# Optimization experiments

Measured on AMD Instinct MI355X. Metric: run time of the kernel, lower is better.

## Reference

```python
import jax, jax.numpy as jnp
import numpy as np
from jax import lax

T, P, EPS = 8, 3, 1e-5


def setup_inputs() -> dict:
    key = jax.random.key(0)
    ks = jax.random.split(key, 12)
    n, c, h, w = 16, 512, 28, 28
    r = c // 8
    sc = 1.0 / np.sqrt(c).astype(np.float32)
    return {
        "X": jax.random.normal(ks[0], (n * T, c, h, w), jnp.float32),
        "conv1_w": jax.random.normal(ks[1], (r, c, 1, 1, 1), jnp.float32) * 0.05,
        "conv1_b": jnp.zeros((r,), jnp.float32),
        "g1": jnp.ones((r,), jnp.float32),
        "b1": jnp.zeros((r,), jnp.float32),
        "m1": jax.random.normal(ks[2], (r,), jnp.float32) * 0.1,
        "v1": jax.random.uniform(ks[3], (r,), jnp.float32, 0.5, 1.5),
        "conv2_w": jax.random.normal(ks[4], (r, r, 3, 1, 1), jnp.float32) * 0.05,
        "conv2_b": jnp.zeros((r,), jnp.float32),
        "conv3_w": jax.random.normal(ks[5], (P, r, 1, 5, 5), jnp.float32) * 0.05,
        "conv3_b": jnp.zeros((P,), jnp.float32),
        "g2": jnp.ones((P,), jnp.float32),
        "b2": jnp.zeros((P,), jnp.float32),
        "m2": jax.random.normal(ks[6], (P,), jnp.float32) * 0.1,
        "v2": jax.random.uniform(ks[7], (P,), jnp.float32, 0.5, 1.5),
        "gcn0_w": jax.random.normal(ks[8], (c, c), jnp.float32) * sc,
        "gcn1_w": jax.random.normal(ks[9], (c, c), jnp.float32) * sc,
        "att_w": jax.random.normal(ks[10], (1, c), jnp.float32) * sc,
        "att_b": jnp.zeros((1,), jnp.float32),
    }


def _conv3d(x, w, b, pad):
    y = lax.conv_general_dilated(x, w, (1, 1, 1), pad,
                                 dimension_numbers=("NCDHW", "OIDHW", "NCDHW"))
    return y + b[None, :, None, None, None]


def _bn(x, g, b, m, v):
    # eval-mode BatchNorm3d folded into scale/shift
    inv = g * lax.rsqrt(v + EPS)
    return x * inv[None, :, None, None, None] + (b - m * inv)[None, :, None, None, None]


def _lrelu(x):
    return jnp.where(x >= 0, x, 0.05 * x)


def reference(X, conv1_w, conv1_b, g1, b1, m1, v1, conv2_w, conv2_b,
              conv3_w, conv3_b, g2, b2, m2, v2, gcn0_w, gcn1_w, att_w, att_b):
    nt, c, h, w = X.shape
    n = nt // T
    Xr = X.reshape(n, T, c, h, w)
    residual = Xr.mean((3, 4))                          # [n,t,c]
    Xp = jnp.transpose(Xr, (0, 2, 1, 3, 4))             # [n,c,t,h,w]

    # saliency detector
    s = _lrelu(_bn(_conv3d(Xp, conv1_w, conv1_b, [(0, 0)] * 3), g1, b1, m1, v1))
    s = _conv3d(s, conv2_w, conv2_b, [(1, 1), (0, 0), (0, 0)])
    s = _conv3d(s, conv3_w, conv3_b, [(0, 0), (2, 2), (2, 2)])
    s_map = jax.nn.sigmoid(_bn(s, g2, b2, m2, v2))      # [n,P,t,h,w]

    # weighted node pooling (avoids the [n,c,P,t,h,w] broadcast intermediate)
    nodes = jnp.einsum('ncthw,npthw->ntpc', Xp, s_map) / (h * w)
    nodes = nodes.reshape(n, T * P, c)                  # [n,N,c], N=24

    # normalized Laplacian as elementwise outer-product scaling
    A = jnp.einsum('nic,njc->nij', nodes, nodes) / c
    deg = jnp.clip(A.sum(-1), 1e-8, None)
    dinv = deg ** -0.5
    L = dinv[:, :, None] * A * dinv[:, None, :]

    # GCN (2 bias-free layers) + attention readout
    Xg = nodes
    for W in (gcn0_w, gcn1_w):
        Xg = _lrelu(L @ (Xg @ W.T))
    att = jax.nn.softmax(L @ ((Xg + nodes) @ att_w.T) + att_b, axis=1)  # [n,N,1]
    readout = (Xg * att).sum(1)                         # [n,c]
    return jnp.concatenate([readout[:, None, :], residual], axis=1)  # [n,t+1,c]
```

## Files before the change

### kernel.cpp

```cpp
#include <hip/hip_runtime.h>
#include <hip/hip_bf16.h>
#include <math.h>

#define NT 128
#define NB 16
#define TT 8
#define C 512
#define RR 64
#define HW 784
#define HH 28
#define WW 28
#define PP 3
#define NN 24
#define EPS 1e-5f

typedef __attribute__((ext_vector_type(8))) short bh8;
typedef __attribute__((ext_vector_type(4))) float f32x4;

static __device__ inline unsigned short f2bf(float f) {
    __hip_bfloat16 h = __float2bfloat16(f);
    return *(unsigned short*)&h;
}
static __device__ inline float bf2f(unsigned short u) {
    __hip_bfloat16 h;
    *(unsigned short*)&h = u;
    return __bfloat162float(h);
}

__global__ __launch_bounds__(256) void convA_mfma(const float* __restrict__ X,
        const float* __restrict__ W1, const float* __restrict__ cb,
        const float* __restrict__ g, const float* __restrict__ bb,
        const float* __restrict__ m, const float* __restrict__ v,
        float* __restrict__ s1)
{
    __shared__ unsigned short Xh[32 * 72];
    __shared__ unsigned short Xl[32 * 72];
    __shared__ unsigned short Wh[4 * 64 * 8];
    __shared__ unsigned short Wl[4 * 64 * 8];
    __shared__ float sInv[64], sAdd[64], sCb[64];

    const int nt  = blockIdx.y;
    const int hw0 = blockIdx.x * 64;
    const int tid = threadIdx.x;

    if (tid < 64) {
        float inv = g[tid] * rsqrtf(v[tid] + EPS);
        sInv[tid] = inv;
        sAdd[tid] = bb[tid] - m[tid] * inv;
        sCb[tid]  = cb[tid];
    }

    const int sk = tid >> 3;
    const int ss = tid & 7;
    const int wr = tid >> 2;
    const int wj = tid & 3;
    const bool full = (hw0 + 64 <= HW);

    const int wv = tid >> 6;
    const int l  = tid & 63;
    const int gq = l >> 4;
    const int mm16 = l & 15;
    const int xbase = (gq * 8) * 72 + 16 * wv + (mm16 ^ ((gq & 1) << 3));

    f32x4 acc[4];
    #pragma unroll
    for (int i = 0; i < 4; ++i) acc[i] = (f32x4){0.f, 0.f, 0.f, 0.f};

    const float* Xnt = X + (size_t)nt * C * HW;

    for (int k0 = 0; k0 < C; k0 += 32) {
        {
            const float* src = Xnt + (size_t)(k0 + sk) * HW + hw0 + ss * 8;
            float x[8];
            if (full) {
                float4 a = *(const float4*)src;
                float4 b = *(const float4*)(src + 4);
                x[0] = a.x; x[1] = a.y; x[2] = a.z; x[3] = a.w;
                x[4] = b.x; x[5] = b.y; x[6] = b.z; x[7] = b.w;
            } else {
                #pragma unroll
                for (int i = 0; i < 8; ++i) {
                    int hw = hw0 + ss * 8 + i;
                    x[i] = (hw < HW) ? src[i] : 0.f;
                }
            }
            unsigned int hp[4], lp[4];
            #pragma unroll
            for (int i = 0; i < 4; ++i) {
                unsigned short h0 = f2bf(x[2 * i]), h1 = f2bf(x[2 * i + 1]);
                unsigned short l0 = f2bf(x[2 * i] - bf2f(h0));
                unsigned short l1 = f2bf(x[2 * i + 1] - bf2f(h1));
                hp[i] = (unsigned int)h0 | ((unsigned int)h1 << 16);
                lp[i] = (unsigned int)l0 | ((unsigned int)l1 << 16);
            }
            int xoff = sk * 72 + ((ss * 8) ^ (((sk >> 3) & 1) << 3));
            *(uint4*)&Xh[xoff] = make_uint4(hp[0], hp[1], hp[2], hp[3]);
            *(uint4*)&Xl[xoff] = make_uint4(lp[0], lp[1], lp[2], lp[3]);
        }
        {
            const float* wsrc = W1 + (size_t)wr * C + k0 + wj * 8;
            float4 a = *(const float4*)wsrc;
            float4 b = *(const float4*)(wsrc + 4);
            float x[8] = {a.x, a.y, a.z, a.w, b.x, b.y, b.z, b.w};
            unsigned int hp[4], lp[4];
            #pragma unroll
            for (int i = 0; i < 4; ++i) {
                unsigned short h0 = f2bf(x[2 * i]), h1 = f2bf(x[2 * i + 1]);
                unsigned short l0 = f2bf(x[2 * i] - bf2f(h0));
                unsigned short l1 = f2bf(x[2 * i + 1] - bf2f(h1));
                hp[i] = (unsigned int)h0 | ((unsigned int)h1 << 16);
                lp[i] = (unsigned int)l0 | ((unsigned int)l1 << 16);
            }
            int woff = ((wr >> 4) * 64 + (wr & 15) + 16 * wj) * 8;
            *(uint4*)&Wh[woff] = make_uint4(hp[0], hp[1], hp[2], hp[3]);
            *(uint4*)&Wl[woff] = make_uint4(lp[0], lp[1], lp[2], lp[3]);
        }
        __syncthreads();

        union { bh8 v; unsigned short u[8]; } fxh, fxl;
        #pragma unroll
        for (int j = 0; j < 8; ++j) {
            fxh.u[j] = Xh[xbase + j * 72];
            fxl.u[j] = Xl[xbase + j * 72];
        }
        #pragma unroll
        for (int rt = 0; rt < 4; ++rt) {
            bh8 wh = *(const bh8*)&Wh[(rt * 64 + l) * 8];
            bh8 wl = *(const bh8*)&Wl[(rt * 64 + l) * 8];
            acc[rt] = __builtin_amdgcn_mfma_f32_16x16x32_bf16(wh, fxh.v, acc[rt], 0, 0, 0);
            acc[rt] = __builtin_amdgcn_mfma_f32_16x16x32_bf16(wh, fxl.v, acc[rt], 0, 0, 0);
            acc[rt] = __builtin_amdgcn_mfma_f32_16x16x32_bf16(wl, fxh.v, acc[rt], 0, 0, 0);
        }
        __syncthreads();
    }

    const int hw = hw0 + 16 * wv + mm16;
    if (hw < HW) {
        #pragma unroll
        for (int rt = 0; rt < 4; ++rt) {
            #pragma unroll
            for (int reg = 0; reg < 4; ++reg) {
                int r = rt * 16 + 4 * gq + reg;
                float y = (acc[rt][reg] + sCb[r]) * sInv[r] + sAdd[r];
                y = (y >= 0.f) ? y : 0.05f * y;
                s1[((size_t)nt * RR + r) * HW + hw] = y;
            }
        }
    }
}

__global__ __launch_bounds__(256) void convB(const float* __restrict__ s1,
        const float* __restrict__ W2, const float* __restrict__ cb,
        float* __restrict__ s2)
{
    __shared__ float Xs[32][64];
    __shared__ float Ws[32][68];
    const int nt = blockIdx.y;
    const int n = nt >> 3, t = nt & 7;
    const int hw0 = blockIdx.x * 64;
    const int tid = threadIdx.x;
    const int tr = tid & 15, tc = tid >> 4;
    float acc[4][4] = {};

    for (int dt = 0; dt < 3; ++dt) {
        int tp = t + dt - 1;
        if (tp < 0 || tp >= TT) continue;
        const float* Sp = s1 + (size_t)(n * TT + tp) * RR * HW;
        for (int k0 = 0; k0 < RR; k0 += 32) {
            #pragma unroll
            for (int i = 0; i < 8; ++i) {
                int idx = tid + i * 256;
                int kl = idx >> 6, hwl = idx & 63;
                int hw = hw0 + hwl;
                Xs[kl][hwl] = (hw < HW) ? Sp[(k0 + kl) * HW + hw] : 0.f;
            }
            #pragma unroll
            for (int i = 0; i < 8; ++i) {
                int idx = tid + i * 256;
                int kl = idx & 31, r = idx >> 5;
                Ws[kl][r] = W2[r * 192 + (k0 + kl) * 3 + dt];
            }
            __syncthreads();
            #pragma unroll
            for (int k = 0; k < 32; ++k) {
                float4 xv = *(const float4*)&Xs[k][tr * 4];
                float4 wv = *(const float4*)&Ws[k][tc * 4];
                acc[0][0] += xv.x * wv.x; acc[0][1] += xv.x * wv.y;
                acc[0][2] += xv.x * wv.z; acc[0][3] += xv.x * wv.w;
                acc[1][0] += xv.y * wv.x; acc[1][1] += xv.y * wv.y;
                acc[1][2] += xv.y * wv.z; acc[1][3] += xv.y * wv.w;
                acc[2][0] += xv.z * wv.x; acc[2][1] += xv.z * wv.y;
                acc[2][2] += xv.z * wv.z; acc[2][3] += xv.z * wv.w;
                acc[3][0] += xv.w * wv.x; acc[3][1] += xv.w * wv.y;
                acc[3][2] += xv.w * wv.z; acc[3][3] += xv.w * wv.w;
            }
            __syncthreads();
        }
    }
    #pragma unroll
    for (int j = 0; j < 4; ++j) {
        int r = tc * 4 + j;
        float cbr = cb[r];
        #pragma unroll
        for (int i = 0; i < 4; ++i) {
            int hw = hw0 + tr * 4 + i;
            if (hw < HW)
                s2[((size_t)nt * RR + r) * HW + hw] = acc[i][j] + cbr;
        }
    }
}

__global__ __launch_bounds__(256) void convC(const float* __restrict__ s2,
        const float* __restrict__ W3, const float* __restrict__ cb,
        const float* __restrict__ g, const float* __restrict__ bb,
        const float* __restrict__ m, const float* __restrict__ v,
        float* __restrict__ smap)
{
    __shared__ float tile[8][18][36];
    const int nt = blockIdx.y;
    const int half = blockIdx.x;
    const int tid = threadIdx.x;
    const int row0 = half * 14 - 2;
    const int orl = tid / 14;
    const int wsi = tid % 14;
    const int orow = half * 14 + orl;
    const int w0 = wsi * 2;
    float acc[3][2] = {};
    const float* S = s2 + (size_t)nt * RR * HW;

    for (int rc0 = 0; rc0 < RR; rc0 += 8) {
        for (int i = 0; i < 21; ++i) {
            int idx = tid + i * 256;
            if (idx < 5184) {
                int rl = idx / 648;
                int rem = idx - rl * 648;
                int rr = rem / 36;
                int cs = rem - rr * 36;
                int grow = row0 + rr;
                int c = cs - 2;
                float val = 0.f;
                if (grow >= 0 && grow < HH && c >= 0 && c < WW)
                    val = S[(rc0 + rl) * HW + grow * WW + c];
                tile[rl][rr][cs] = val;
            }
        }
        __syncthreads();
        if (tid < 196) {
            #pragma unroll
            for (int rl = 0; rl < 8; ++rl) {
                const float* wr2 = W3 + (rc0 + rl) * 25;
                #pragma unroll
                for (int dh = 0; dh < 5; ++dh) {
                    const float* trow = &tile[rl][orl + dh][w0];
                    float inb[6];
                    #pragma unroll
                    for (int q = 0; q < 6; ++q) inb[q] = trow[q];
                    #pragma unroll
                    for (int dw = 0; dw < 5; ++dw) {
                        float v0 = inb[dw], v1 = inb[dw + 1];
                        #pragma unroll
                        for (int p = 0; p < 3; ++p) {
                            float wv = wr2[p * 1600 + dh * 5 + dw];
                            acc[p][0] += v0 * wv;
                            acc[p][1] += v1 * wv;
                        }
                    }
                }
            }
        }
        __syncthreads();
    }
    if (tid < 196) {
        #pragma unroll
        for (int p = 0; p < 3; ++p) {
            float inv = g[p] / sqrtf(v[p] + EPS);
            float add = bb[p] - m[p] * inv;
            #pragma unroll
            for (int j = 0; j < 2; ++j) {
                float z = (acc[p][j] + cb[p]) * inv + add;
                float sg = 1.f / (1.f + expf(-z));
                smap[((size_t)nt * PP + p) * HW + orow * WW + w0 + j] = sg;
            }
        }
    }
}

__global__ __launch_bounds__(256) void poolD(const float* __restrict__ X,
        const float* __restrict__ smap, float* __restrict__ nodes,
        float* __restrict__ out)
{
    const int tid = threadIdx.x;
    const int lane = tid & 63;
    const int gw = blockIdx.x * 4 + (tid >> 6);
    const int c = gw & 511;
    const int nt = gw >> 9;
    const float4* X4 = (const float4*)(X + ((size_t)nt * C + c) * HW);
    const float4* S0 = (const float4*)(smap + (size_t)nt * PP * HW);
    const float4* S1 = S0 + 196;
    const float4* S2 = S1 + 196;
    float sx = 0.f, a0 = 0.f, a1 = 0.f, a2 = 0.f;
    #pragma unroll
    for (int i = 0; i < 4; ++i) {
        int fi = i * 64 + lane;
        if (fi < 196) {
            float4 x = X4[fi];
            float4 p0 = S0[fi], p1 = S1[fi], p2 = S2[fi];
            sx += x.x + x.y + x.z + x.w;
            a0 += x.x * p0.x + x.y * p0.y + x.z * p0.z + x.w * p0.w;
            a1 += x.x * p1.x + x.y * p1.y + x.z * p1.z + x.w * p1.w;
            a2 += x.x * p2.x + x.y * p2.y + x.z * p2.z + x.w * p2.w;
        }
    }
    #pragma unroll
    for (int off = 32; off >= 1; off >>= 1) {
        sx += __shfl_xor(sx, off);
        a0 += __shfl_xor(a0, off);
        a1 += __shfl_xor(a1, off);
        a2 += __shfl_xor(a2, off);
    }
    if (lane == 0) {
        int n = nt >> 3, t = nt & 7;
        const float s = 1.f / 784.f;
        out[((size_t)n * 9 + 1 + t) * C + c] = sx * s;
        float* nd = nodes + ((size_t)n * NN + t * PP) * C + c;
        nd[0]     = a0 * s;
        nd[C]     = a1 * s;
        nd[2 * C] = a2 * s;
    }
}

__global__ __launch_bounds__(256) void graphL(const float* __restrict__ nodes,
        float* __restrict__ Lg)
{
    __shared__ float4 nds[24][129];
    __shared__ float Amat[24][24];
    __shared__ float dinv[24];
    const int n = blockIdx.x;
    const int tid = threadIdx.x;
    const float4* src = (const float4*)(nodes + (size_t)n * NN * C);
    #pragma unroll
    for (int i = 0; i < 12; ++i) {
        int fi = tid + i * 256;
        int row = fi >> 7, k4 = fi & 127;
        nds[row][k4] = src[row * 128 + k4];
    }
    __syncthreads();
    for (int pair = tid; pair < 576; pair += 256) {
        int i = pair / 24, j = pair - (pair / 24) * 24;
        const float4* ri = &nds[i][0];
        const float4* rj = &nds[j][0];
        float s = 0.f;
        for (int k = 0; k < 128; ++k) {
            float4 a = ri[k], b = rj[k];
            s += a.x * b.x + a.y * b.y + a.z * b.z + a.w * b.w;
        }
        Amat[i][j] = s * (1.f / 512.f);
    }
    __syncthreads();
    if (tid < 24) {
        float d = 0.f;
        for (int j = 0; j < 24; ++j) d += Amat[tid][j];
        d = fmaxf(d, 1e-8f);
        dinv[tid] = 1.f / sqrtf(d);
    }
    __syncthreads();
    for (int pair = tid; pair < 576; pair += 256) {
        int i = pair / 24, j = pair - (pair / 24) * 24;
        Lg[(size_t)n * 576 + pair] = dinv[i] * Amat[i][j] * dinv[j];
    }
}

__global__ __launch_bounds__(256) void gemmG(const float* __restrict__ Xin,
        const float* __restrict__ Wm, float* __restrict__ Y)
{
    __shared__ float Xs[32][36];
    __shared__ float Ws[32][66];
    const int o0 = blockIdx.x * 64;
    const int m0 = blockIdx.y * 32;
    const int tid = threadIdx.x;
    const int tr = tid >> 5;
    const int tc = tid & 31;
    float acc[4][2] = {};

    for (int k0 = 0; k0 < 512; k0 += 32) {
        {
            int ml = tid >> 3, k4 = tid & 7;
            float4 xv = *(const float4*)&Xin[(size_t)(m0 + ml) * 512 + k0 + k4 * 4];
            Xs[k4 * 4 + 0][ml] = xv.x; Xs[k4 * 4 + 1][ml] = xv.y;
            Xs[k4 * 4 + 2][ml] = xv.z; Xs[k4 * 4 + 3][ml] = xv.w;
        }
        #pragma unroll
        for (int i = 0; i < 2; ++i) {
            int idx = tid + i * 256;
            int ol = idx >> 3, k4 = idx & 7;
            float4 wv = *(const float4*)&Wm[(size_t)(o0 + ol) * 512 + k0 + k4 * 4];
            Ws[k4 * 4 + 0][ol] = wv.x; Ws[k4 * 4 + 1][ol] = wv.y;
            Ws[k4 * 4 + 2][ol] = wv.z; Ws[k4 * 4 + 3][ol] = wv.w;
        }
        __syncthreads();
        #pragma unroll
        for (int k = 0; k < 32; ++k) {
            float4 xv = *(const float4*)&Xs[k][tr * 4];
            float2 wv = *(const float2*)&Ws[k][tc * 2];
            acc[0][0] += xv.x * wv.x; acc[0][1] += xv.x * wv.y;
            acc[1][0] += xv.y * wv.x; acc[1][1] += xv.y * wv.y;
            acc[2][0] += xv.z * wv.x; acc[2][1] += xv.z * wv.y;
            acc[3][0] += xv.w * wv.x; acc[3][1] += xv.w * wv.y;
        }
        __syncthreads();
    }
    #pragma unroll
    for (int i2 = 0; i2 < 4; ++i2)
        #pragma unroll
        for (int j = 0; j < 2; ++j)
            Y[(size_t)(m0 + tr * 4 + i2) * 512 + o0 + tc * 2 + j] = acc[i2][j];
}

__global__ __launch_bounds__(256) void applyL(const float* __restrict__ G,
        const float* __restrict__ Lg, float* __restrict__ Xg)
{
    __shared__ float Ls[576];
    const int n = blockIdx.y;
    const int tid = threadIdx.x;
    for (int i = tid; i < 576; i += 256) Ls[i] = Lg[(size_t)n * 576 + i];
    __syncthreads();
    const int o = blockIdx.x * 128 + (tid & 127);
    const int ig = (tid >> 7) * 12;
    float acc[12] = {};
    const float* Gn = G + (size_t)n * NN * 512;
    for (int j = 0; j < 24; ++j) {
        float gv = Gn[j * 512 + o];
        #pragma unroll
        for (int i = 0; i < 12; ++i)
            acc[i] += Ls[(ig + i) * 24 + j] * gv;
    }
    float* Xn = Xg + (size_t)n * NN * 512;
    #pragma unroll
    for (int i = 0; i < 12; ++i) {
        float y = acc[i];
        Xn[(ig + i) * 512 + o] = (y >= 0.f) ? y : 0.05f * y;
    }
}

__global__ __launch_bounds__(256) void attE(const float* __restrict__ Xg,
        const float* __restrict__ nodes, const float* __restrict__ Lg,
        const float* __restrict__ aw, const float* __restrict__ ab,
        float* __restrict__ out)
{
    __shared__ float zs[24], ys[24], att[24], Ls[576];
    const int n = blockIdx.x;
    const int tid = threadIdx.x;
    const int lane = tid & 63, wv = tid >> 6;
    for (int i = tid; i < 576; i += 256) Ls[i] = Lg[(size_t)n * 576 + i];
    const float* Xn = Xg + (size_t)n * NN * 512;
    const float* Nn = nodes + (size_t)n * NN * 512;
    for (int i = wv; i < 24; i += 4) {
        float s = 0.f;
        #pragma unroll
        for (int kk = 0; kk < 8; ++kk) {
            int k = kk * 64 + lane;
            s += (Xn[i * 512 + k] + Nn[i * 512 + k]) * aw[k];
        }
        #pragma unroll
        for (int off = 32; off >= 1; off >>= 1) s += __shfl_xor(s, off);
        if (lane == 0) zs[i] = s;
    }
    __syncthreads();
    if (tid < 24) {
        float y = ab[0];
        for (int j = 0; j < 24; ++j) y += Ls[tid * 24 + j] * zs[j];
        ys[tid] = y;
    }
    __syncthreads();
    if (tid < 64) {
        float vv = (tid < 24) ? ys[tid] : -3.4e38f;
        float mx = vv;
        #pragma unroll
        for (int off = 32; off >= 1; off >>= 1) mx = fmaxf(mx, __shfl_xor(mx, off));
        float e = (tid < 24) ? expf(vv - mx) : 0.f;
        float ssum = e;
        #pragma unroll
        for (int off = 32; off >= 1; off >>= 1) ssum += __shfl_xor(ssum, off);
        if (tid < 24) att[tid] = e / ssum;
    }
    __syncthreads();
    for (int c2 = tid; c2 < 512; c2 += 256) {
        float r = 0.f;
        #pragma unroll
        for (int i = 0; i < 24; ++i) r += Xn[i * 512 + c2] * att[i];
        out[(size_t)n * 9 * 512 + c2] = r;
    }
}

extern "C" void kernel_launch(void* const* d_in, const int* in_sizes, int n_in,
                              void* d_out, int out_size, void* d_ws, size_t ws_size,
                              hipStream_t stream)
{
    const float* X   = (const float*)d_in[0];
    const float* w1  = (const float*)d_in[1];
    const float* b1c = (const float*)d_in[2];
    const float* g1  = (const float*)d_in[3];
    const float* b1  = (const float*)d_in[4];
    const float* m1  = (const float*)d_in[5];
    const float* v1  = (const float*)d_in[6];
    const float* w2  = (const float*)d_in[7];
    const float* b2c = (const float*)d_in[8];
    const float* w3  = (const float*)d_in[9];
    const float* b3c = (const float*)d_in[10];
    const float* g2  = (const float*)d_in[11];
    const float* b2  = (const float*)d_in[12];
    const float* m2  = (const float*)d_in[13];
    const float* v2  = (const float*)d_in[14];
    const float* gw0 = (const float*)d_in[15];
    const float* gw1 = (const float*)d_in[16];
    const float* aw  = (const float*)d_in[17];
    const float* ab  = (const float*)d_in[18];
    float* out = (float*)d_out;

    float* ws    = (float*)d_ws;
    float* s1    = ws;
    float* s2    = s1 + (size_t)NT * RR * HW;
    float* smap  = s2 + (size_t)NT * RR * HW;
    float* nodes = smap + (size_t)NT * PP * HW;
    float* Lg    = nodes + (size_t)NB * NN * C;
    float* gt    = Lg + (size_t)NB * NN * NN;
    float* xa    = gt + (size_t)NB * NN * C;
    float* xb    = xa + (size_t)NB * NN * C;

    convA_mfma<<<dim3(13, NT), 256, 0, stream>>>(X, w1, b1c, g1, b1, m1, v1, s1);
    convB<<<dim3(13, NT), 256, 0, stream>>>(s1, w2, b2c, s2);
    convC<<<dim3(2, NT), 256, 0, stream>>>(s2, w3, b3c, g2, b2, m2, v2, smap);
    poolD<<<dim3(16384), 256, 0, stream>>>(X, smap, nodes, out);
    graphL<<<dim3(NB), 256, 0, stream>>>(nodes, Lg);
    gemmG<<<dim3(8, 12), 256, 0, stream>>>(nodes, gw0, gt);
    applyL<<<dim3(4, NB), 256, 0, stream>>>(gt, Lg, xa);
    gemmG<<<dim3(8, 12), 256, 0, stream>>>(xa, gw1, gt);
    applyL<<<dim3(4, NB), 256, 0, stream>>>(gt, Lg, xb);
    attE<<<dim3(NB), 256, 0, stream>>>(xb, nodes, Lg, aw, ab, out);
}
```

Measured before the change: 599.3 us.

## Move temporal conv to split-bf16 MFMA and restructure 5x5 conv as channel-split sliding window

```diff
diff --git a/kernel.cpp b/kernel.cpp
--- a/kernel.cpp
+++ b/kernel.cpp
@@ -16,14 +16,15 @@
 
 typedef __attribute__((ext_vector_type(8))) short bh8;
 typedef __attribute__((ext_vector_type(4))) float f32x4;
-
-static __device__ inline unsigned short f2bf(float f) {
+typedef unsigned short u16;
+
+static __device__ inline u16 f2bf(float f) {
     __hip_bfloat16 h = __float2bfloat16(f);
-    return *(unsigned short*)&h;
-}
-static __device__ inline float bf2f(unsigned short u) {
+    return *(u16*)&h;
+}
+static __device__ inline float bf2f(u16 u) {
     __hip_bfloat16 h;
-    *(unsigned short*)&h = u;
+    *(u16*)&h = u;
     return __bfloat162float(h);
 }
 
@@ -31,12 +32,12 @@
         const float* __restrict__ W1, const float* __restrict__ cb,
         const float* __restrict__ g, const float* __restrict__ bb,
         const float* __restrict__ m, const float* __restrict__ v,
-        float* __restrict__ s1)
-{
-    __shared__ unsigned short Xh[32 * 72];
-    __shared__ unsigned short Xl[32 * 72];
-    __shared__ unsigned short Wh[4 * 64 * 8];
-    __shared__ unsigned short Wl[4 * 64 * 8];
+        u16* __restrict__ s1h, u16* __restrict__ s1l)
+{
+    __shared__ u16 Xh[32 * 72];
+    __shared__ u16 Xl[32 * 72];
+    __shared__ u16 Wh[4 * 64 * 8];
+    __shared__ u16 Wl[4 * 64 * 8];
     __shared__ float sInv[64], sAdd[64], sCb[64];
 
     const int nt  = blockIdx.y;
@@ -87,9 +88,9 @@
             unsigned int hp[4], lp[4];
             #pragma unroll
             for (int i = 0; i < 4; ++i) {
-                unsigned short h0 = f2bf(x[2 * i]), h1 = f2bf(x[2 * i + 1]);
-                unsigned short l0 = f2bf(x[2 * i] - bf2f(h0));
-                unsigned short l1 = f2bf(x[2 * i + 1] - bf2f(h1));
+                u16 h0 = f2bf(x[2 * i]), h1 = f2bf(x[2 * i + 1]);
+                u16 l0 = f2bf(x[2 * i] - bf2f(h0));
+                u16 l1 = f2bf(x[2 * i + 1] - bf2f(h1));
                 hp[i] = (unsigned int)h0 | ((unsigned int)h1 << 16);
                 lp[i] = (unsigned int)l0 | ((unsigned int)l1 << 16);
             }
@@ -105,9 +106,9 @@
             unsigned int hp[4], lp[4];
             #pragma unroll
             for (int i = 0; i < 4; ++i) {
-                unsigned short h0 = f2bf(x[2 * i]), h1 = f2bf(x[2 * i + 1]);
-                unsigned short l0 = f2bf(x[2 * i] - bf2f(h0));
-                unsigned short l1 = f2bf(x[2 * i + 1] - bf2f(h1));
+                u16 h0 = f2bf(x[2 * i]), h1 = f2bf(x[2 * i + 1]);
+                u16 l0 = f2bf(x[2 * i] - bf2f(h0));
+                u16 l1 = f2bf(x[2 * i + 1] - bf2f(h1));
                 hp[i] = (unsigned int)h0 | ((unsigned int)h1 << 16);
                 lp[i] = (unsigned int)l0 | ((unsigned int)l1 << 16);
             }
@@ -117,7 +118,7 @@
         }
         __syncthreads();
 
-        union { bh8 v; unsigned short u[8]; } fxh, fxl;
+        union { bh8 v; u16 u[8]; } fxh, fxl;
         #pragma unroll
         for (int j = 0; j < 8; ++j) {
             fxh.u[j] = Xh[xbase + j * 72];
@@ -143,146 +144,213 @@
                 int r = rt * 16 + 4 * gq + reg;
                 float y = (acc[rt][reg] + sCb[r]) * sInv[r] + sAdd[r];
                 y = (y >= 0.f) ? y : 0.05f * y;
-                s1[((size_t)nt * RR + r) * HW + hw] = y;
-            }
-        }
-    }
-}
-
-__global__ __launch_bounds__(256) void convB(const float* __restrict__ s1,
-        const float* __restrict__ W2, const float* __restrict__ cb,
-        float* __restrict__ s2)
-{
-    __shared__ float Xs[32][64];
-    __shared__ float Ws[32][68];
-    const int nt = blockIdx.y;
+                size_t idx = ((size_t)nt * RR + r) * HW + hw;
+                u16 h = f2bf(y);
+                s1h[idx] = h;
+                s1l[idx] = f2bf(y - bf2f(h));
+            }
+        }
+    }
+}
+
+__global__ __launch_bounds__(256) void convB_mfma(const u16* __restrict__ s1h,
+        const u16* __restrict__ s1l, const float* __restrict__ W2,
+        const float* __restrict__ cb, float* __restrict__ s2)
+{
+    __shared__ u16 Xh[32 * 72];
+    __shared__ u16 Xl[32 * 72];
+    __shared__ u16 Wh[6 * 4 * 64 * 8];
+    __shared__ u16 Wl[6 * 4 * 64 * 8];
+
+    const int nt  = blockIdx.y;
     const int n = nt >> 3, t = nt & 7;
     const int hw0 = blockIdx.x * 64;
     const int tid = threadIdx.x;
-    const int tr = tid & 15, tc = tid >> 4;
-    float acc[4][4] = {};
+    const bool full = (hw0 + 64 <= HW);
+
+    const int wr = tid >> 2, wj = tid & 3;
+    #pragma unroll
+    for (int dk = 0; dk < 6; ++dk) {
+        int dt = dk >> 1, kc = dk & 1;
+        const float* wsrc = W2 + (size_t)wr * 192 + (kc * 32 + wj * 8) * 3 + dt;
+        float x[8];
+        #pragma unroll
+        for (int i = 0; i < 8; ++i) x[i] = wsrc[i * 3];
+        unsigned int hp[4], lp[4];
+        #pragma unroll
+        for (int i = 0; i < 4; ++i) {
+            u16 h0 = f2bf(x[2 * i]), h1 = f2bf(x[2 * i + 1]);
+            u16 l0 = f2bf(x[2 * i] - bf2f(h0));
+            u16 l1 = f2bf(x[2 * i + 1] - bf2f(h1));
+            hp[i] = (unsigned int)h0 | ((unsigned int)h1 << 16);
+            lp[i] = (unsigned int)l0 | ((unsigned int)l1 << 16);
+        }
+        int woff = dk * 2048 + ((wr >> 4) * 64 + (wr & 15) + 16 * wj) * 8;
+        *(uint4*)&Wh[woff] = make_uint4(hp[0], hp[1], hp[2], hp[3]);
+        *(uint4*)&Wl[woff] = make_uint4(lp[0], lp[1], lp[2], lp[3]);
+    }
+    __syncthreads();
+
+    const int sk = tid >> 3, ss = tid & 7;
+    const int wv = tid >> 6, l = tid & 63;
+    const int gq = l >> 4, mm16 = l & 15;
+    const int xbase = (gq * 8) * 72 + 16 * wv + (mm16 ^ ((gq & 1) << 3));
+    const int xoff = sk * 72 + ((ss * 8) ^ (((sk >> 3) & 1) << 3));
+
+    f32x4 acc[4];
+    #pragma unroll
+    for (int i = 0; i < 4; ++i) acc[i] = (f32x4){0.f, 0.f, 0.f, 0.f};
 
     for (int dt = 0; dt < 3; ++dt) {
         int tp = t + dt - 1;
         if (tp < 0 || tp >= TT) continue;
-        const float* Sp = s1 + (size_t)(n * TT + tp) * RR * HW;
-        for (int k0 = 0; k0 < RR; k0 += 32) {
-            #pragma unroll
-            for (int i = 0; i < 8; ++i) {
-                int idx = tid + i * 256;
-                int kl = idx >> 6, hwl = idx & 63;
-                int hw = hw0 + hwl;
-                Xs[kl][hwl] = (hw < HW) ? Sp[(k0 + kl) * HW + hw] : 0.f;
-            }
-            #pragma unroll
-            for (int i = 0; i < 8; ++i) {
-                int idx = tid + i * 256;
-                int kl = idx & 31, r = idx >> 5;
-                Ws[kl][r] = W2[r * 192 + (k0 + kl) * 3 + dt];
+        const size_t pbase = (size_t)(n * TT + tp) * RR * HW;
+        #pragma unroll
+        for (int kc = 0; kc < 2; ++kc) {
+            const size_t roff = pbase + (size_t)(kc * 32 + sk) * HW + hw0 + ss * 8;
+            uint4 hv, lv;
+            if (full) {
+                hv = *(const uint4*)(s1h + roff);
+                lv = *(const uint4*)(s1l + roff);
+            } else {
+                u16 ha[8], la[8];
+                #pragma unroll
+                for (int i = 0; i < 8; ++i) {
+                    int hw = hw0 + ss * 8 + i;
+                    ha[i] = (hw < HW) ? s1h[roff + i] : (u16)0;
+                    la[i] = (hw < HW) ? s1l[roff + i] : (u16)0;
+                }
+                hv = *(uint4*)ha; lv = *(uint4*)la;
             }
             __syncthreads();
-            #pragma unroll
-            for (int k = 0; k < 32; ++k) {
-                float4 xv = *(const float4*)&Xs[k][tr * 4];
-                float4 wv = *(const float4*)&Ws[k][tc * 4];
-                acc[0][0] += xv.x * wv.x; acc[0][1] += xv.x * wv.y;
-                acc[0][2] += xv.x * wv.z; acc[0][3] += xv.x * wv.w;
-                acc[1][0] += xv.y * wv.x; acc[1][1] += xv.y * wv.y;
-                acc[1][2] += xv.y * wv.z; acc[1][3] += xv.y * wv.w;
-                acc[2][0] += xv.z * wv.x; acc[2][1] += xv.z * wv.y;
-                acc[2][2] += xv.z * wv.z; acc[2][3] += xv.z * wv.w;
-                acc[3][0] += xv.w * wv.x; acc[3][1] += xv.w * wv.y;
-                acc[3][2] += xv.w * wv.z; acc[3][3] += xv.w * wv.w;
-            }
+            *(uint4*)&Xh[xoff] = hv;
+            *(uint4*)&Xl[xoff] = lv;
             __syncthreads();
-        }
-    }
-    #pragma unroll
-    for (int j = 0; j < 4; ++j) {
-        int r = tc * 4 + j;
-        float cbr = cb[r];
-        #pragma unroll
-        for (int i = 0; i < 4; ++i) {
-            int hw = hw0 + tr * 4 + i;
-            if (hw < HW)
-                s2[((size_t)nt * RR + r) * HW + hw] = acc[i][j] + cbr;
-        }
-    }
-}
-
-__global__ __launch_bounds__(256) void convC(const float* __restrict__ s2,
-        const float* __restrict__ W3, const float* __restrict__ cb,
-        const float* __restrict__ g, const float* __restrict__ bb,
-        const float* __restrict__ m, const float* __restrict__ v,
-        float* __restrict__ smap)
-{
-    __shared__ float tile[8][18][36];
-    const int nt = blockIdx.y;
-    const int half = blockIdx.x;
-    const int tid = threadIdx.x;
-    const int row0 = half * 14 - 2;
-    const int orl = tid / 14;
-    const int wsi = tid % 14;
-    const int orow = half * 14 + orl;
-    const int w0 = wsi * 2;
-    float acc[3][2] = {};
-    const float* S = s2 + (size_t)nt * RR * HW;
-
-    for (int rc0 = 0; rc0 < RR; rc0 += 8) {
-        for (int i = 0; i < 21; ++i) {
-            int idx = tid + i * 256;
-            if (idx < 5184) {
-                int rl = idx / 648;
-                int rem = idx - rl * 648;
-                int rr = rem / 36;
-                int cs = rem - rr * 36;
-                int grow = row0 + rr;
-                int c = cs - 2;
-                float val = 0.f;
-                if (grow >= 0 && grow < HH && c >= 0 && c < WW)
-                    val = S[(rc0 + rl) * HW + grow * WW + c];
-                tile[rl][rr][cs] = val;
-            }
-        }
-        __syncthreads();
-        if (tid < 196) {
-            #pragma unroll
-            for (int rl = 0; rl < 8; ++rl) {
-                const float* wr2 = W3 + (rc0 + rl) * 25;
+
+            union { bh8 v; u16 u[8]; } fxh, fxl;
+            #pragma unroll
+            for (int j = 0; j < 8; ++j) {
+                fxh.u[j] = Xh[xbase + j * 72];
+                fxl.u[j] = Xl[xbase + j * 72];
+            }
+            const int dk = dt * 2 + kc;
+            #pragma unroll
+            for (int rt = 0; rt < 4; ++rt) {
+                bh8 wh = *(const bh8*)&Wh[dk * 2048 + (rt * 64 + l) * 8];
+                bh8 wl = *(const bh8*)&Wl[dk * 2048 + (rt * 64 + l) * 8];
+                acc[rt] = __builtin_amdgcn_mfma_f32_16x16x32_bf16(wh, fxh.v, acc[rt], 0, 0, 0);
+                acc[rt] = __builtin_amdgcn_mfma_f32_16x16x32_bf16(wh, fxl.v, acc[rt], 0, 0, 0);
+                acc[rt] = __builtin_amdgcn_mfma_f32_16x16x32_bf16(wl, fxh.v, acc[rt], 0, 0, 0);
+            }
+        }
+    }
+
+    const int hw = hw0 + 16 * wv + mm16;
+    if (hw < HW) {
+        #pragma unroll
+        for (int rt = 0; rt < 4; ++rt) {
+            #pragma unroll
+            for (int reg = 0; reg < 4; ++reg) {
+                int r = rt * 16 + 4 * gq + reg;
+                s2[((size_t)nt * RR + r) * HW + hw] = acc[rt][reg] + cb[r];
+            }
+        }
+    }
+}
+
+__global__ __launch_bounds__(256) void convC_sw(const float* __restrict__ s2,
+        const float* __restrict__ W3, float* __restrict__ partial)
+{
+    const int tid  = threadIdx.x;
+    const int wave = tid >> 6;
+    const int lane = tid & 63;
+    const int half = lane >> 5;
+    const int col  = lane & 31;
+    const int item = blockIdx.x * 8 + wave * 2 + half;
+    const int band = item & 3;
+    const int nt   = (item >> 2) & 127;
+    int cg = item >> 9;
+    cg = __builtin_amdgcn_readfirstlane(cg);
+
+    const int row0 = band * 7;
+    const bool cok = (col < 28);
+
+    float acc[3][7];
+    #pragma unroll
+    for (int p = 0; p < 3; ++p)
+        #pragma unroll
+        for (int r = 0; r < 7; ++r) acc[p][r] = 0.f;
+
+    for (int chi = 0; chi < 8; ++chi) {
+        float wgt[75];
+        #pragma unroll
+        for (int p = 0; p < 3; ++p)
+            #pragma unroll
+            for (int q = 0; q < 25; ++q)
+                wgt[p * 25 + q] = W3[(size_t)(p * 64 + cg * 8 + chi) * 25 + q];
+
+        const float* src = s2 + ((size_t)nt * RR + cg * 8 + chi) * HW;
+        float w[5][5];
+
+        #pragma unroll
+        for (int rr = 0; rr < 4; ++rr) {
+            int R = row0 - 2 + rr;
+            bool rok = (R >= 0) & (R < HH);
+            #pragma unroll
+            for (int j = 0; j < 5; ++j) {
+                int cc = col - 2 + j;
+                bool ok = rok & cok & (cc >= 0) & (cc < WW);
+                w[rr][j] = ok ? src[R * WW + cc] : 0.f;
+            }
+        }
+        #pragma unroll
+        for (int r = 0; r < 7; ++r) {
+            {
+                int R = row0 + 2 + r;
+                bool rok = (R < HH);
+                int slot = (r + 4) % 5;
                 #pragma unroll
-                for (int dh = 0; dh < 5; ++dh) {
-                    const float* trow = &tile[rl][orl + dh][w0];
-                    float inb[6];
+                for (int j = 0; j < 5; ++j) {
+                    int cc = col - 2 + j;
+                    bool ok = rok & cok & (cc >= 0) & (cc < WW);
+                    w[slot][j] = ok ? src[R * WW + cc] : 0.f;
+                }
+            }
+            #pragma unroll
+            for (int p = 0; p < 3; ++p)
+                #pragma unroll
+                for (int dh = 0; dh < 5; ++dh)
                     #pragma unroll
-                    for (int q = 0; q < 6; ++q) inb[q] = trow[q];
-                    #pragma unroll
-                    for (int dw = 0; dw < 5; ++dw) {
-                        float v0 = inb[dw], v1 = inb[dw + 1];
-                        #pragma unroll
-                        for (int p = 0; p < 3; ++p) {
-                            float wv = wr2[p * 1600 + dh * 5 + dw];
-                            acc[p][0] += v0 * wv;
-                            acc[p][1] += v1 * wv;
-                        }
-                    }
-                }
-            }
-        }
-        __syncthreads();
-    }
-    if (tid < 196) {
-        #pragma unroll
-        for (int p = 0; p < 3; ++p) {
-            float inv = g[p] / sqrtf(v[p] + EPS);
-            float add = bb[p] - m[p] * inv;
-            #pragma unroll
-            for (int j = 0; j < 2; ++j) {
-                float z = (acc[p][j] + cb[p]) * inv + add;
-                float sg = 1.f / (1.f + expf(-z));
-                smap[((size_t)nt * PP + p) * HW + orow * WW + w0 + j] = sg;
-            }
-        }
-    }
+                    for (int dw = 0; dw < 5; ++dw)
+                        acc[p][r] += w[(r + dh) % 5][dw] * wgt[p * 25 + dh * 5 + dw];
+        }
+    }
+
+    if (cok) {
+        #pragma unroll
+        for (int p = 0; p < 3; ++p)
+            #pragma unroll
+            for (int r = 0; r < 7; ++r)
+                partial[(((size_t)cg * 128 + nt) * 3 + p) * HW + (row0 + r) * WW + col]
+                    = acc[p][r];
+    }
+}
+
+__global__ __launch_bounds__(256) void convC_fin(const float* __restrict__ partial,
+        const float* __restrict__ cb, const float* __restrict__ g,
+        const float* __restrict__ bb, const float* __restrict__ m,
+        const float* __restrict__ v, float* __restrict__ smap)
+{
+    const int idx = blockIdx.x * 256 + threadIdx.x;
+    const int total = 128 * 3 * HW;
+    if (idx >= total) return;
+    const int p = (idx / HW) % 3;
+    float a = cb[p];
+    #pragma unroll
+    for (int gg = 0; gg < 8; ++gg) a += partial[(size_t)gg * total + idx];
+    float inv = g[p] * rsqrtf(v[p] + EPS);
+    float z = a * inv + (bb[p] - m[p] * inv);
+    smap[idx] = 1.f / (1.f + expf(-z));
 }
 
 __global__ __launch_bounds__(256) void poolD(const float* __restrict__ X,
@@ -517,19 +585,22 @@
     const float* ab  = (const float*)d_in[18];
     float* out = (float*)d_out;
 
-    float* ws    = (float*)d_ws;
-    float* s1    = ws;
-    float* s2    = s1 + (size_t)NT * RR * HW;
-    float* smap  = s2 + (size_t)NT * RR * HW;
+    const size_t S1N = (size_t)NT * RR * HW;
+    u16*   s1h   = (u16*)d_ws;
+    u16*   s1l   = s1h + S1N;
+    float* part  = (float*)d_ws;
+    float* s2    = (float*)(s1l + S1N);
+    float* smap  = s2 + S1N;
     float* nodes = smap + (size_t)NT * PP * HW;
     float* Lg    = nodes + (size_t)NB * NN * C;
     float* gt    = Lg + (size_t)NB * NN * NN;
     float* xa    = gt + (size_t)NB * NN * C;
     float* xb    = xa + (size_t)NB * NN * C;
 
-    convA_mfma<<<dim3(13, NT), 256, 0, stream>>>(X, w1, b1c, g1, b1, m1, v1, s1);
-    convB<<<dim3(13, NT), 256, 0, stream>>>(s1, w2, b2c, s2);
-    convC<<<dim3(2, NT), 256, 0, stream>>>(s2, w3, b3c, g2, b2, m2, v2, smap);
+    convA_mfma<<<dim3(13, NT), 256, 0, stream>>>(X, w1, b1c, g1, b1, m1, v1, s1h, s1l);
+    convB_mfma<<<dim3(13, NT), 256, 0, stream>>>(s1h, s1l, w2, b2c, s2);
+    convC_sw<<<dim3(512), 256, 0, stream>>>(s2, w3, part);
+    convC_fin<<<dim3(1176), 256, 0, stream>>>(part, b3c, g2, b2, m2, v2, smap);
     poolD<<<dim3(16384), 256, 0, stream>>>(X, smap, nodes, out);
     graphL<<<dim3(NB), 256, 0, stream>>>(nodes, Lg);
     gemmG<<<dim3(8, 12), 256, 0, stream>>>(nodes, gw0, gt);
```

After: 498.3 us. 16.9% less time.
